# Kernel tuning notes

Hardware: AMD Instinct MI355X
Metric: run time of the kernel (lower is better)

## Reference

```python
import jax, jax.numpy as jnp
import numpy as np

SL, BS, D = 2048, 2, 1024
H, DH = 16, 64  # num_heads, nhid

def setup_inputs() -> dict:
    key = jax.random.key(0)
    ks = jax.random.split(key, 8)
    inv = 1.0 / np.sqrt(D)
    return {
        "query": jax.random.normal(ks[0], (SL, BS, D), jnp.float32),
        "keys": jax.random.normal(ks[1], (SL, BS, D), jnp.float32),
        "values": jax.random.normal(ks[2], (SL, BS, D), jnp.float32),
        "mask": jnp.ones((1, 1, SL, SL), jnp.int32),
        "Wq": jax.random.normal(ks[3], (H * DH, D), jnp.float32) * inv,
        "Wk": jax.random.normal(ks[4], (H * DH, D), jnp.float32) * inv,
        "Wv": jax.random.normal(ks[5], (H * DH, D), jnp.float32) * inv,
        "Wo": jax.random.normal(ks[6], (D, H * DH), jnp.float32) * inv,
    }

def reference(query, keys, values, mask, Wq, Wk, Wv, Wo):
    slq, bs, _ = query.shape
    sl = keys.shape[0]
    # nn.Linear(bias=False): x @ W.T ; then view to (s, b, H, DH)
    q = (query @ Wq.T).reshape(slq, bs, H, DH)   # sbhd
    k = (keys @ Wk.T).reshape(sl, bs, H, DH)
    v = (values @ Wv.T).reshape(sl, bs, H, DH)
    # NOTE: original forward never applies self.scale -> unscaled scores.
    scores = jnp.einsum('qbhd,kbhd->bhqk', q, k)
    scores = jnp.where(mask == 0, jnp.float32(-1e20), scores)
    weights = jax.nn.softmax(scores, axis=-1)
    attn = jnp.einsum('bhqk,kbhd->qbhd', weights, v).reshape(slq, bs, H * DH)
    return attn @ Wo.T  # [slq, bs, out_dim]
```

## Files before the change

kernel.cpp:

```cpp
#include <hip/hip_runtime.h>


typedef __attribute__((ext_vector_type(4))) float  f32x4;
typedef __attribute__((ext_vector_type(8))) __bf16 bf16x8;
typedef __attribute__((ext_vector_type(4))) __bf16 bf16x4;
typedef __attribute__((ext_vector_type(4))) short  s16x4;

#define SLEN 2048
#define BSZ  2
#define DMODEL 1024
#define NHEAD 16
#define DHEAD 64
#define D3 (3 * DMODEL)

__device__ __forceinline__ void async16(void* lds, const void* g) {
    __builtin_amdgcn_global_load_lds(
        (const __attribute__((address_space(1))) unsigned int*)g,
        (__attribute__((address_space(3))) unsigned int*)lds, 16, 0, 0);
}

__device__ __forceinline__ f32x4 mfma16(bf16x8 a, bf16x8 b, f32x4 c) {
    return __builtin_amdgcn_mfma_f32_16x16x32_bf16(a, b, c, 0, 0, 0);
}

__device__ __forceinline__ f32x4 mfma16k16(bf16x4 a, bf16x4 b, f32x4 c) {
#if __has_builtin(__builtin_amdgcn_mfma_f32_16x16x16_bf16)
    return __builtin_amdgcn_mfma_f32_16x16x16_bf16(a, b, c, 0, 0, 0);
#else
    return __builtin_amdgcn_mfma_f32_16x16x16bf16_1k(
        __builtin_bit_cast(s16x4, a), __builtin_bit_cast(s16x4, b), c, 0, 0, 0);
#endif
}

struct CvtArgs {
    const float* src[7];
    __bf16* dst[7];
    int n4[7];
    float scale[7];
    const int* mask;
    unsigned int* flag;
    int maskn4;
};
__global__ void cvt_all(CvtArgs a) {
    const int t = blockIdx.y;
    const int stride = gridDim.x * blockDim.x;
    if (t == 7) {
        bool ok = true;
        for (int i = blockIdx.x * blockDim.x + threadIdx.x; i < a.maskn4; i += stride) {
            int4 v = ((const int4*)a.mask)[i];
            ok = ok && v.x && v.y && v.z && v.w;
        }
        if (!ok) atomicAnd(a.flag, 0u);
        return;
    }
    const float* __restrict__ src = a.src[t];
    __bf16* __restrict__ dst = a.dst[t];
    const int n4 = a.n4[t];
    const float sc = a.scale[t];
    for (int i = blockIdx.x * blockDim.x + threadIdx.x; i < n4; i += stride) {
        float4 v = ((const float4*)src)[i];
        bf16x4 o;
        o[0] = (__bf16)(v.x * sc); o[1] = (__bf16)(v.y * sc);
        o[2] = (__bf16)(v.z * sc); o[3] = (__bf16)(v.w * sc);
        ((bf16x4*)dst)[i] = o;
    }
}

__global__ __launch_bounds__(256, 3) void gemm_qkv(const __bf16* __restrict__ Xq,
                                                   const __bf16* __restrict__ Xk,
                                                   const __bf16* __restrict__ Xv,
                                                   const __bf16* __restrict__ W,
                                                   __bf16* __restrict__ C) {
    __shared__ __bf16 At[128 * 64];
    __shared__ __bf16 Bt[128 * 64];
    const int tid = threadIdx.x;
    const int lane = tid & 63, wv = tid >> 6;
    const int l15 = lane & 15, l4 = lane >> 4;
    const int wr = wv >> 1, wc = wv & 1;
    const int srow = lane >> 3;
    const int sbyte = (((lane & 7) ^ srow) << 4);
    const int bm = blockIdx.x, bn = blockIdx.y;
    const __bf16* A = (bn < 8) ? Xq : (bn < 16) ? Xk : Xv;
    const char* Ab = (const char*)(A + (size_t)bm * 128 * DMODEL);
    const char* Bb = (const char*)(W + (size_t)bn * 128 * DMODEL);

    f32x4 acc[4][4];
#pragma unroll
    for (int m = 0; m < 4; m++)
#pragma unroll
        for (int n = 0; n < 4; n++)
#pragma unroll
            for (int r = 0; r < 4; r++) acc[m][n][r] = 0.0f;

    for (int k0 = 0; k0 < DMODEL; k0 += 64) {
        __syncthreads();
#pragma unroll
        for (int i = 0; i < 8; i++) {
            int c = wv * 8 + i;
            if (c < 16) {
                int row = c * 8 + srow;
                async16(&At[c * 512], Ab + ((size_t)row * DMODEL + k0) * 2 + sbyte);
            } else {
                int row = (c - 16) * 8 + srow;
                async16(&Bt[(c - 16) * 512], Bb + ((size_t)row * DMODEL + k0) * 2 + sbyte);
            }
        }
        __syncthreads();

#pragma unroll
        for (int kk = 0; kk < 2; kk++) {
            bf16x8 af[4], bfr[4];
#pragma unroll
            for (int m = 0; m < 4; m++) {
                int row = wr * 64 + m * 16 + l15;
                int col = (kk * 32 + l4 * 8) ^ ((row & 7) << 3);
                af[m] = *(const bf16x8*)&At[row * 64 + col];
            }
#pragma unroll
            for (int n = 0; n < 4; n++) {
                int row = wc * 64 + n * 16 + l15;
                int col = (kk * 32 + l4 * 8) ^ ((row & 7) << 3);
                bfr[n] = *(const bf16x8*)&Bt[row * 64 + col];
            }
#pragma unroll
            for (int m = 0; m < 4; m++)
#pragma unroll
                for (int n = 0; n < 4; n++)
                    acc[m][n] = mfma16(af[m], bfr[n], acc[m][n]);
        }
    }

#pragma unroll
    for (int m = 0; m < 4; m++)
#pragma unroll
        for (int n = 0; n < 4; n++)
#pragma unroll
            for (int r = 0; r < 4; r++) {
                size_t row = (size_t)bm * 128 + wr * 64 + m * 16 + l4 * 4 + r;
                size_t col = (size_t)bn * 128 + wc * 64 + n * 16 + l15;
                C[row * D3 + col] = (__bf16)acc[m][n][r];
            }
}

__global__ __launch_bounds__(256, 2) void gemm_out(const __bf16* __restrict__ A,
                                                   const __bf16* __restrict__ B,
                                                   float* __restrict__ Cv) {
    __shared__ __bf16 At[2][128 * 64];
    __shared__ __bf16 Bt[2][64 * 64];
    const int tid = threadIdx.x;
    const int lane = tid & 63, wv = tid >> 6;
    const int l15 = lane & 15, l4 = lane >> 4;
    const int wr = wv >> 1, wc = wv & 1;
    const int srow = lane >> 3;
    const int sbyte = (((lane & 7) ^ srow) << 4);
    const int bm = blockIdx.x, bn = blockIdx.y;
    const char* Ab = (const char*)(A + (size_t)bm * 128 * DMODEL);
    const char* Bb = (const char*)(B + (size_t)bn * 64 * DMODEL);

    f32x4 acc[4][2];
#pragma unroll
    for (int m = 0; m < 4; m++)
#pragma unroll
        for (int n = 0; n < 2; n++)
#pragma unroll
            for (int r = 0; r < 4; r++) acc[m][n][r] = 0.0f;

    auto stage = [&](int buf, int k0) {
#pragma unroll
        for (int i = 0; i < 6; i++) {
            int c = wv * 6 + i;
            if (c < 16) {
                int row = c * 8 + srow;
                async16(&At[buf][c * 512], Ab + ((size_t)row * DMODEL + k0) * 2 + sbyte);
            } else {
                int row = (c - 16) * 8 + srow;
                async16(&Bt[buf][(c - 16) * 512], Bb + ((size_t)row * DMODEL + k0) * 2 + sbyte);
            }
        }
    };

    stage(0, 0);
    __syncthreads();
    int cur = 0;
    for (int k0 = 0; k0 < DMODEL; k0 += 64) {
        if (k0 + 64 < DMODEL) stage(cur ^ 1, k0 + 64);
#pragma unroll
        for (int kk = 0; kk < 2; kk++) {
            bf16x8 af[4], bfr[2];
#pragma unroll
            for (int m = 0; m < 4; m++) {
                int row = wr * 64 + m * 16 + l15;
                int col = (kk * 32 + l4 * 8) ^ ((row & 7) << 3);
                af[m] = *(const bf16x8*)&At[cur][row * 64 + col];
            }
#pragma unroll
            for (int n = 0; n < 2; n++) {
                int row = wc * 32 + n * 16 + l15;
                int col = (kk * 32 + l4 * 8) ^ ((row & 7) << 3);
                bfr[n] = *(const bf16x8*)&Bt[cur][row * 64 + col];
            }
#pragma unroll
            for (int m = 0; m < 4; m++)
#pragma unroll
                for (int n = 0; n < 2; n++)
                    acc[m][n] = mfma16(af[m], bfr[n], acc[m][n]);
        }
        __syncthreads();
        cur ^= 1;
    }

#pragma unroll
    for (int m = 0; m < 4; m++)
#pragma unroll
        for (int n = 0; n < 2; n++)
#pragma unroll
            for (int r = 0; r < 4; r++) {
                size_t row = (size_t)bm * 128 + wr * 64 + m * 16 + l4 * 4 + r;
                size_t col = (size_t)bn * 64 + wc * 32 + n * 16 + l15;
                Cv[row * DMODEL + col] = acc[m][n][r];
            }
}

__global__ __launch_bounds__(256) void transpose_v(const __bf16* __restrict__ QKV,
                                                   __bf16* __restrict__ Vt) {
    __shared__ __bf16 t[64][72];
    const int stile = blockIdx.x;
    const int bh = blockIdx.y;
    const int b = bh >> 4, h = bh & 15;
    const int tid = threadIdx.x;
    {
        int sr = tid >> 2, d0 = (tid & 3) * 16;
        const __bf16* src = QKV + ((size_t)((stile * 64 + sr) * BSZ + b) * D3 + 2 * DMODEL + h * 64 + d0);
        *(bf16x8*)&t[sr][d0]     = *(const bf16x8*)src;
        *(bf16x8*)&t[sr][d0 + 8] = *(const bf16x8*)(src + 8);
    }
    __syncthreads();
    {
        int d = tid >> 2, n = tid & 3;
        int s0 = n * 16;
        __bf16* dst = Vt + ((size_t)(bh * 64 + d) * SLEN + stile * 64);
#pragma unroll
        for (int l4g = 0; l4g < 4; l4g++) {
            bf16x4 w;
#pragma unroll
            for (int r = 0; r < 4; r++) w[r] = t[s0 + l4g * 4 + r][d];
            *(bf16x4*)(dst + l4g * 16 + n * 4) = w;
        }
    }
}

__global__ __launch_bounds__(256, 2) void attn_fwd(const __bf16* __restrict__ QKV,
                                                   const __bf16* __restrict__ Vt,
                                                   const int* __restrict__ mask,
                                                   const unsigned int* __restrict__ flag,
                                                   __bf16* __restrict__ Attn) {
    __shared__ __bf16 Kt[2][2][64 * 64];
    __shared__ __bf16 Vs[2][2][64 * 64];
    const int tid = threadIdx.x;
    const int lane = tid & 63, wv = tid >> 6;
    const int l15 = lane & 15, l4 = lane >> 4;
    const int blk = blockIdx.x;
    const int xcd = blk & 7, idx = blk >> 3;
    const int bh = xcd + (idx >> 4) * 8;
    const int qt = idx & 15;
    const int b = bh >> 4, h = bh & 15;
    const bool allones = (*flag != 0u);
    const int srow = lane >> 3;
    const int sbyte = (((lane & 7) ^ srow) << 4);

    bf16x8 aq[2][2];
#pragma unroll
    for (int m = 0; m < 2; m++)
#pragma unroll
        for (int kk = 0; kk < 2; kk++) {
            int qrow = qt * 128 + wv * 32 + m * 16 + l15;
            aq[m][kk] = *(const bf16x8*)(QKV + ((size_t)(qrow * BSZ + b) * D3 + h * 64 + kk * 32 + l4 * 8));
        }

    f32x4 o[2][4];
    float lr[2];
#pragma unroll
    for (int m = 0; m < 2; m++) {
#pragma unroll
        for (int nd = 0; nd < 4; nd++)
#pragma unroll
            for (int r = 0; r < 4; r++) o[m][nd][r] = 0.0f;
        lr[m] = 0.0f;
    }

    const char* Kb = (const char*)QKV + ((size_t)b * D3 + DMODEL + h * 64) * 2;
    const char* Vb = (const char*)Vt + ((size_t)bh * 64) * SLEN * 2;

    auto stage = [&](int buf, int kt) {
#pragma unroll
        for (int i = 0; i < 8; i++) {
            int c = wv * 8 + i;
            if (c < 16) {
                int kh = c >> 3, ck = c & 7;
                int krow = kt * 128 + kh * 64 + ck * 8 + srow;
                async16(&Kt[buf][kh][ck * 512],
                        Kb + (size_t)krow * (BSZ * D3 * 2) + sbyte);
            } else {
                int c2 = c - 16;
                int kh = c2 >> 3, ck = c2 & 7;
                int drow = ck * 8 + srow;
                async16(&Vs[buf][kh][ck * 512],
                        Vb + (size_t)drow * (SLEN * 2) + kt * 256 + kh * 128 + sbyte);
            }
        }
    };

    stage(0, 0);
    __syncthreads();
    int cur = 0;

    for (int kt = 0; kt < SLEN / 128; kt++) {
        if (kt + 1 < SLEN / 128) stage(cur ^ 1, kt + 1);

#pragma unroll
        for (int kh = 0; kh < 2; kh++) {
            const __bf16* Kl = Kt[cur][kh];
            const __bf16* Vl = Vs[cur][kh];

            bf16x8 bk[4][2];
#pragma unroll
            for (int n = 0; n < 4; n++) {
                int row = n * 16 + l15;
#pragma unroll
                for (int kk = 0; kk < 2; kk++) {
                    int col = (kk * 32 + l4 * 8) ^ ((row & 7) << 3);
                    bk[n][kk] = *(const bf16x8*)&Kl[row * 64 + col];
                }
            }

            f32x4 s[2][4];
#pragma unroll
            for (int m = 0; m < 2; m++)
#pragma unroll
                for (int n = 0; n < 4; n++)
#pragma unroll
                    for (int r = 0; r < 4; r++) s[m][n][r] = 0.0f;
            __builtin_amdgcn_s_setprio(1);
#pragma unroll
            for (int n = 0; n < 4; n++)
#pragma unroll
                for (int kk = 0; kk < 2; kk++)
#pragma unroll
                    for (int m = 0; m < 2; m++)
                        s[m][n] = mfma16(bk[n][kk], aq[m][kk], s[m][n]);
            __builtin_amdgcn_s_setprio(0);

            if (!allones) {
#pragma unroll
                for (int m = 0; m < 2; m++) {
                    int q = qt * 128 + wv * 32 + m * 16 + l15;
#pragma unroll
                    for (int n = 0; n < 4; n++)
#pragma unroll
                        for (int r = 0; r < 4; r++) {
                            int kg = kt * 128 + kh * 64 + n * 16 + l4 * 4 + r;
                            if (mask[(size_t)q * SLEN + kg] == 0) s[m][n][r] = -1e20f;
                        }
                }
            }

            bf16x4 pb[2][4];
#pragma unroll
            for (int m = 0; m < 2; m++)
#pragma unroll
                for (int n = 0; n < 4; n++) {
                    float p0 = __builtin_amdgcn_exp2f(s[m][n][0]);
                    float p1 = __builtin_amdgcn_exp2f(s[m][n][1]);
                    float p2 = __builtin_amdgcn_exp2f(s[m][n][2]);
                    float p3 = __builtin_amdgcn_exp2f(s[m][n][3]);
                    lr[m] += (p0 + p1) + (p2 + p3);
                    bf16x4 w;
                    w[0] = (__bf16)p0; w[1] = (__bf16)p1;
                    w[2] = (__bf16)p2; w[3] = (__bf16)p3;
                    pb[m][n] = w;
                }

            bf16x8 avv[4][2];
#pragma unroll
            for (int nd = 0; nd < 4; nd++) {
                int row = nd * 16 + l15;
#pragma unroll
                for (int hh = 0; hh < 2; hh++) {
                    int col = (l4 * 16 + hh * 8) ^ ((row & 7) << 3);
                    avv[nd][hh] = *(const bf16x8*)&Vl[row * 64 + col];
                }
            }

            __builtin_amdgcn_s_setprio(1);
#pragma unroll
            for (int n = 0; n < 4; n++) {
#pragma unroll
                for (int nd = 0; nd < 4; nd++) {
                    bf16x4 av = (n & 1)
                        ? __builtin_shufflevector(avv[nd][n >> 1], avv[nd][n >> 1], 4, 5, 6, 7)
                        : __builtin_shufflevector(avv[nd][n >> 1], avv[nd][n >> 1], 0, 1, 2, 3);
#pragma unroll
                    for (int m = 0; m < 2; m++)
                        o[m][nd] = mfma16k16(av, pb[m][n], o[m][nd]);
                }
            }
            __builtin_amdgcn_s_setprio(0);
        }

        __syncthreads();
        cur ^= 1;
    }

#pragma unroll
    for (int m = 0; m < 2; m++) {
        lr[m] += __shfl_xor(lr[m], 16);
        lr[m] += __shfl_xor(lr[m], 32);
    }

#pragma unroll
    for (int m = 0; m < 2; m++) {
        float inv = 1.0f / lr[m];
        int qrow = qt * 128 + wv * 32 + m * 16 + l15;
#pragma unroll
        for (int nd = 0; nd < 4; nd++) {
            bf16x4 ov;
#pragma unroll
            for (int r = 0; r < 4; r++) ov[r] = (__bf16)(o[m][nd][r] * inv);
            *(bf16x4*)(Attn + ((size_t)(qrow * BSZ + b)) * DMODEL + h * 64 + nd * 16 + l4 * 4) = ov;
        }
    }
}

extern "C" void kernel_launch(void* const* d_in, const int* in_sizes, int n_in,
                              void* d_out, int out_size, void* d_ws, size_t ws_size,
                              hipStream_t stream) {
    const float* query  = (const float*)d_in[0];
    const float* keys   = (const float*)d_in[1];
    const float* values = (const float*)d_in[2];
    const int*   mask   = (const int*)d_in[3];
    const float* Wq     = (const float*)d_in[4];
    const float* Wk     = (const float*)d_in[5];
    const float* Wv     = (const float*)d_in[6];
    const float* Wo     = (const float*)d_in[7];
    float* out = (float*)d_out;

    char* ws = (char*)d_ws;
    const size_t MB = 1024 * 1024;
    __bf16* XQ   = (__bf16*)(ws + 0);
    __bf16* XK   = (__bf16*)(ws + 8 * MB);
    __bf16* XV   = (__bf16*)(ws + 16 * MB);
    __bf16* WCAT = (__bf16*)(ws + 24 * MB);
    __bf16* WQB  = WCAT;
    __bf16* WKB  = (__bf16*)(ws + 26 * MB);
    __bf16* WVB  = (__bf16*)(ws + 28 * MB);
    __bf16* WOB  = (__bf16*)(ws + 30 * MB);
    __bf16* QKV  = (__bf16*)(ws + 32 * MB);
    __bf16* VT   = (__bf16*)(ws + 0);
    __bf16* ATT  = (__bf16*)(ws + 8 * MB);
    unsigned int* flag = (unsigned int*)(ws + 56 * MB);

    (void)hipMemsetAsync(flag, 0xFF, 4, stream);

    const int NTOK = SLEN * BSZ;
    const int NBIG = NTOK * DMODEL / 4, NW = DMODEL * DMODEL / 4;
    const float LOG2E = 1.4426950408889634f;
    CvtArgs ca;
    ca.src[0] = query;  ca.dst[0] = XQ;  ca.n4[0] = NBIG; ca.scale[0] = 1.0f;
    ca.src[1] = keys;   ca.dst[1] = XK;  ca.n4[1] = NBIG; ca.scale[1] = 1.0f;
    ca.src[2] = values; ca.dst[2] = XV;  ca.n4[2] = NBIG; ca.scale[2] = 1.0f;
    ca.src[3] = Wq;     ca.dst[3] = WQB; ca.n4[3] = NW;   ca.scale[3] = LOG2E;
    ca.src[4] = Wk;     ca.dst[4] = WKB; ca.n4[4] = NW;   ca.scale[4] = 1.0f;
    ca.src[5] = Wv;     ca.dst[5] = WVB; ca.n4[5] = NW;   ca.scale[5] = 1.0f;
    ca.src[6] = Wo;     ca.dst[6] = WOB; ca.n4[6] = NW;   ca.scale[6] = 1.0f;
    ca.mask = mask; ca.flag = flag; ca.maskn4 = SLEN * SLEN / 4;
    cvt_all<<<dim3(256, 8), 256, 0, stream>>>(ca);

    gemm_qkv<<<dim3(NTOK / 128, D3 / 128), 256, 0, stream>>>(XQ, XK, XV, WCAT, QKV);

    transpose_v<<<dim3(SLEN / 64, BSZ * NHEAD), 256, 0, stream>>>(QKV, VT);

    attn_fwd<<<BSZ * NHEAD * (SLEN / 128), 256, 0, stream>>>(QKV, VT, mask, flag, ATT);

    gemm_out<<<dim3(NTOK / 128, DMODEL / 64), 256, 0, stream>>>(ATT, WOB, out);
}
```

Baseline: 132.2 us.

## Permute K row staging so PV uses 16x16x32 MFMA instead of 16x16x16

```diff
diff --git a/kernel.cpp b/kernel.cpp
--- a/kernel.cpp
+++ b/kernel.cpp
@@ -4,7 +4,6 @@
 typedef __attribute__((ext_vector_type(4))) float  f32x4;
 typedef __attribute__((ext_vector_type(8))) __bf16 bf16x8;
 typedef __attribute__((ext_vector_type(4))) __bf16 bf16x4;
-typedef __attribute__((ext_vector_type(4))) short  s16x4;
 
 #define SLEN 2048
 #define BSZ  2
@@ -21,15 +20,6 @@
 
 __device__ __forceinline__ f32x4 mfma16(bf16x8 a, bf16x8 b, f32x4 c) {
     return __builtin_amdgcn_mfma_f32_16x16x32_bf16(a, b, c, 0, 0, 0);
-}
-
-__device__ __forceinline__ f32x4 mfma16k16(bf16x4 a, bf16x4 b, f32x4 c) {
-#if __has_builtin(__builtin_amdgcn_mfma_f32_16x16x16_bf16)
-    return __builtin_amdgcn_mfma_f32_16x16x16_bf16(a, b, c, 0, 0, 0);
-#else
-    return __builtin_amdgcn_mfma_f32_16x16x16bf16_1k(
-        __builtin_bit_cast(s16x4, a), __builtin_bit_cast(s16x4, b), c, 0, 0, 0);
-#endif
 }
 
 struct CvtArgs {
@@ -236,16 +226,13 @@
     }
     __syncthreads();
     {
-        int d = tid >> 2, n = tid & 3;
-        int s0 = n * 16;
-        __bf16* dst = Vt + ((size_t)(bh * 64 + d) * SLEN + stile * 64);
-#pragma unroll
-        for (int l4g = 0; l4g < 4; l4g++) {
-            bf16x4 w;
-#pragma unroll
-            for (int r = 0; r < 4; r++) w[r] = t[s0 + l4g * 4 + r][d];
-            *(bf16x4*)(dst + l4g * 16 + n * 4) = w;
-        }
+        int d = tid >> 2, s0 = (tid & 3) * 16;
+        bf16x8 o1, o2;
+#pragma unroll
+        for (int j = 0; j < 8; j++) { o1[j] = t[s0 + j][d]; o2[j] = t[s0 + 8 + j][d]; }
+        __bf16* dst = Vt + ((size_t)(bh * 64 + d) * SLEN + stile * 64 + s0);
+        *(bf16x8*)dst = o1;
+        *(bf16x8*)(dst + 8) = o2;
     }
 }
 
@@ -297,7 +284,9 @@
             int c = wv * 8 + i;
             if (c < 16) {
                 int kh = c >> 3, ck = c & 7;
-                int krow = kt * 128 + kh * 64 + ck * 8 + srow;
+                int p = (ck & 7) * 8 + srow;
+                int kperm = (p & 32) + ((p & 12) << 1) + (((p >> 4) & 1) << 2) + (p & 3);
+                int krow = kt * 128 + kh * 64 + kperm;
                 async16(&Kt[buf][kh][ck * 512],
                         Kb + (size_t)krow * (BSZ * D3 * 2) + sbyte);
             } else {
@@ -358,50 +347,37 @@
                     for (int n = 0; n < 4; n++)
 #pragma unroll
                         for (int r = 0; r < 4; r++) {
-                            int kg = kt * 128 + kh * 64 + n * 16 + l4 * 4 + r;
+                            int kg = kt * 128 + kh * 64 + (n >> 1) * 32 + l4 * 8 + (n & 1) * 4 + r;
                             if (mask[(size_t)q * SLEN + kg] == 0) s[m][n][r] = -1e20f;
                         }
                 }
             }
 
-            bf16x4 pb[2][4];
+            bf16x8 pb8[2][2];
 #pragma unroll
             for (int m = 0; m < 2; m++)
 #pragma unroll
-                for (int n = 0; n < 4; n++) {
-                    float p0 = __builtin_amdgcn_exp2f(s[m][n][0]);
-                    float p1 = __builtin_amdgcn_exp2f(s[m][n][1]);
-                    float p2 = __builtin_amdgcn_exp2f(s[m][n][2]);
-                    float p3 = __builtin_amdgcn_exp2f(s[m][n][3]);
-                    lr[m] += (p0 + p1) + (p2 + p3);
-                    bf16x4 w;
-                    w[0] = (__bf16)p0; w[1] = (__bf16)p1;
-                    w[2] = (__bf16)p2; w[3] = (__bf16)p3;
-                    pb[m][n] = w;
-                }
-
-            bf16x8 avv[4][2];
-#pragma unroll
-            for (int nd = 0; nd < 4; nd++) {
-                int row = nd * 16 + l15;
-#pragma unroll
-                for (int hh = 0; hh < 2; hh++) {
-                    int col = (l4 * 16 + hh * 8) ^ ((row & 7) << 3);
-                    avv[nd][hh] = *(const bf16x8*)&Vl[row * 64 + col];
-                }
-            }
+                for (int half = 0; half < 2; half++)
+#pragma unroll
+                    for (int nn = 0; nn < 2; nn++)
+#pragma unroll
+                        for (int r = 0; r < 4; r++) {
+                            float p = __builtin_amdgcn_exp2f(s[m][half * 2 + nn][r]);
+                            lr[m] += p;
+                            pb8[m][half][nn * 4 + r] = (__bf16)p;
+                        }
 
             __builtin_amdgcn_s_setprio(1);
 #pragma unroll
-            for (int n = 0; n < 4; n++) {
+            for (int half = 0; half < 2; half++) {
 #pragma unroll
                 for (int nd = 0; nd < 4; nd++) {
-                    bf16x4 av = (n & 1)
-                        ? __builtin_shufflevector(avv[nd][n >> 1], avv[nd][n >> 1], 4, 5, 6, 7)
-                        : __builtin_shufflevector(avv[nd][n >> 1], avv[nd][n >> 1], 0, 1, 2, 3);
+                    int row = nd * 16 + l15;
+                    int col = (half * 32 + l4 * 8) ^ ((row & 7) << 3);
+                    bf16x8 av = *(const bf16x8*)&Vl[row * 64 + col];
 #pragma unroll
                     for (int m = 0; m < 2; m++)
-                        o[m][nd] = mfma16k16(av, pb[m][n], o[m][nd]);
+                        o[m][nd] = mfma16(av, pb8[m][half], o[m][nd]);
                 }
             }
             __builtin_amdgcn_s_setprio(0);
```

New measurement: 122.9 us. 7.0% less time.
